# Performance work log

Hardware: AMD Instinct MI355X
Metric: run time of the kernel (lower is better)

The kernel has to match this reference:

```python
import jax, jax.numpy as jnp
from jax import lax
import numpy as np

NH = 4                      # num_heads in CrossScaleCom
KS = [3, 5, 7, 9]           # per-head depthwise kernel sizes
WS = 2                      # window_size in LocalFeatureGuided
GGM_K = 7                   # guide-token generator kernel size


def _dwconv(x, w, stride, pad):
    # depthwise conv: w has shape (C, 1, k, k), feature_group_count = C
    return lax.conv_general_dilated(
        x, w, (stride, stride), [(pad, pad), (pad, pad)],
        feature_group_count=x.shape[1],
        dimension_numbers=("NCHW", "OIHW", "NCHW"))


def _forward(x, dw_w0, dw_b0, dw_w1, dw_b1, dw_w2, dw_b2, dw_w3, dw_b3,
             csc_w, csc_b, bn_gamma, bn_beta, bn_mean, bn_var,
             ggm_w, ggm_b, qkv_w, qkv_b, proj_w, proj_b):
    B, C, H, W = x.shape
    cph = C // NH
    # ---- CrossScaleCom: per-head multi-scale depthwise convs ----
    xh = x.reshape(B, NH, cph, H, W)
    dws = [(dw_w0, dw_b0), (dw_w1, dw_b1), (dw_w2, dw_b2), (dw_w3, dw_b3)]
    heads = [_dwconv(xh[:, i], w, 1, KS[i] // 2) + b[None, :, None, None]
             for i, (w, b) in enumerate(dws)]
    y = jnp.stack(heads, 1)                      # (B, NH, cph, H, W)
    y = y.transpose(0, 2, 1, 3, 4).reshape(B, C, H, W)  # channel shuffle
    y = jnp.einsum("bchw,oc->bohw", y, csc_w) + csc_b[None, :, None, None]
    Co = y.shape[1]
    # ---- LocalFeatureGuided ----
    # ggm: BatchNorm (eval) -> GELU (exact) -> depthwise conv k=7 stride=WS
    inv = bn_gamma / jnp.sqrt(bn_var + 1e-5)
    g = (y - bn_mean[None, :, None, None]) * inv[None, :, None, None] \
        + bn_beta[None, :, None, None]
    g = jax.nn.gelu(g, approximate=False)
    g = _dwconv(g, ggm_w, WS, GGM_K // 2) + ggm_b[None, :, None, None]  # (B,Co,Ho,Wo)
    Ho, Wo = H // WS, W // WS
    L = Ho * Wo
    # unfold(kernel=WS, stride=WS) -> (B, Co, WS*WS, L), torch unfold ordering
    xu = y.reshape(B, Co, Ho, WS, Wo, WS).transpose(0, 1, 3, 5, 2, 4)
    xu = xu.reshape(B, Co, WS * WS, L)
    tokens = jnp.concatenate([g.reshape(B, Co, 1, L), xu], axis=2)  # (B,Co,5,L)
    # 1x1 conv over channel dim == einsum
    qkv = jnp.einsum("bcpl,oc->bopl", tokens, qkv_w) + qkv_b[None, :, None, None]
    q, k, v = jnp.split(qkv, 3, axis=1)          # each (B, Co, 5, L)
    # tiny 5x5 attention per (batch, channel), contracting over windows L
    attn = jnp.einsum("bcpl,bcql->bcpq", q, k) / (Co ** 0.5)
    attn = jax.nn.softmax(attn, axis=-1)
    out = jnp.einsum("bcpq,bcql->bcpl", attn, v)  # (B, Co, 5, L)
    out = out[:, :, 0, :].reshape(B, Co, Ho, Wo)  # guide-token output
    out = jnp.einsum("bchw,oc->bohw", out, proj_w) + proj_b[None, :, None, None]
    return out


def setup_inputs() -> dict:
    key = jax.random.key(0)
    ks = jax.random.split(key, 16)
    B, Cin, Cout, H, W = 8, 64, 128, 224, 224
    cph = Cin // NH
    s = 0.05
    d = {"x": jax.random.normal(ks[0], (B, Cin, H, W), jnp.float32)}
    for i, kk in enumerate(KS):
        d[f"dw_w{i}"] = jax.random.normal(ks[1 + i], (cph, 1, kk, kk), jnp.float32) * s
        d[f"dw_b{i}"] = jnp.zeros((cph,), jnp.float32)
    d["csc_w"] = jax.random.normal(ks[5], (Cout, Cin), jnp.float32) * s
    d["csc_b"] = jnp.zeros((Cout,), jnp.float32)
    d["bn_gamma"] = jnp.ones((Cout,), jnp.float32)
    d["bn_beta"] = jnp.zeros((Cout,), jnp.float32)
    d["bn_mean"] = jnp.zeros((Cout,), jnp.float32)
    d["bn_var"] = jnp.ones((Cout,), jnp.float32)
    d["ggm_w"] = jax.random.normal(ks[6], (Cout, 1, GGM_K, GGM_K), jnp.float32) * s
    d["ggm_b"] = jnp.zeros((Cout,), jnp.float32)
    d["qkv_w"] = jax.random.normal(ks[7], (3 * Cout, Cout), jnp.float32) * s
    d["qkv_b"] = jnp.zeros((3 * Cout,), jnp.float32)
    d["proj_w"] = jax.random.normal(ks[8], (Cout, Cout), jnp.float32) * s
    d["proj_b"] = jnp.zeros((Cout,), jnp.float32)
    return d


def reference(x, dw_w0, dw_b0, dw_w1, dw_b1, dw_w2, dw_b2, dw_w3, dw_b3,
              csc_w, csc_b, bn_gamma, bn_beta, bn_mean, bn_var,
              ggm_w, ggm_b, qkv_w, qkv_b, proj_w, proj_b):
    return _forward(x, dw_w0, dw_b0, dw_w1, dw_b1, dw_w2, dw_b2, dw_w3, dw_b3,
                    csc_w, csc_b, bn_gamma, bn_beta, bn_mean, bn_var,
                    ggm_w, ggm_b, qkv_w, qkv_b, proj_w, proj_b)
```

## Files before the change

kernel.cpp:

```cpp
#include <hip/hip_runtime.h>

#define BB 8
#define CIN 64
#define CO 128
#define Hdim 224
#define Wdim 224
#define HWt (224*224)
#define HO 112
#define WO 112
#define Lt (112*112)

typedef unsigned short u16;
typedef short bf16x8 __attribute__((ext_vector_type(8)));
typedef float f32x4  __attribute__((ext_vector_type(4)));
#define MFMA16(a,b,c) __builtin_amdgcn_mfma_f32_16x16x32_bf16((a),(b),(c),0,0,0)

__device__ inline u16 f2bf(float f) {
    union { float f; unsigned u; } v; v.f = f;
    unsigned r = (v.u + 0x7fffu + ((v.u >> 16) & 1u)) >> 16;
    return (u16)r;
}
__device__ inline float bf2f(u16 h) {
    union { unsigned u; float f; } v; v.u = ((unsigned)h) << 16; return v.f;
}
__device__ inline float uasf(unsigned u) {
    union { unsigned u; float f; } v; v.u = u; return v.f;
}
__device__ inline float sum8bf(uint4 v) {
    return bf2f(v.x & 0xffff) + bf2f(v.x >> 16) + bf2f(v.y & 0xffff) + bf2f(v.y >> 16)
         + bf2f(v.z & 0xffff) + bf2f(v.z >> 16) + bf2f(v.w & 0xffff) + bf2f(v.w >> 16);
}

__device__ inline float gelu_fast(float x) {
    float z  = x * 0.7071067811865476f;
    float az = fabsf(z);
    float t  = __builtin_amdgcn_rcpf(fmaf(0.3275911f, az, 1.0f));
    float p  = fmaf(fmaf(fmaf(fmaf(1.061405429f, t, -1.453152027f), t,
                    1.421413741f), t, -0.284496736f), t, 0.254829592f);
    float e  = __expf(-z * z);
    float er = copysignf(1.0f - p * t * e, z);
    return 0.5f * x * (1.0f + er);
}

template<int HEAD>
__global__ __launch_bounds__(256) void dw_conv(
    const float* __restrict__ x, const float* __restrict__ w,
    const float* __restrict__ bias, u16* __restrict__ dwb)
{
    constexpr int K   = 3 + 2*HEAD;
    constexpr int PAD = HEAD + 1;
    constexpr int R   = 32 + 2*PAD;
    const int tile = blockIdx.x;
    const int c    = blockIdx.y;
    const int b    = blockIdx.z;
    const int th = (tile/7)*32, tw = (tile%7)*32;
    __shared__ float patch[R*40];
    const int tid = threadIdx.x;
    const float* xin = x + (size_t)(b*CIN + HEAD*16 + c)*HWt;
    for (int idx = tid; idx < R*40; idx += 256) {
        int r = idx / 40, cc = idx - r*40;
        int gy = th - PAD + r, gx = tw - 4 + cc;
        float v = 0.f;
        if (gy >= 0 && gy < Hdim && gx >= 0 && gx < Wdim) v = xin[gy*Wdim + gx];
        patch[idx] = v;
    }
    float wreg[K*K];
    const float* wp = w + c*K*K;
    #pragma unroll
    for (int i = 0; i < K*K; i++) wreg[i] = wp[i];
    const float bv = bias[c];
    __syncthreads();

    const int ty = tid >> 3, x0 = (tid & 7) * 4;
    float acc[4] = {bv, bv, bv, bv};
    #pragma unroll
    for (int ky = 0; ky < K; ky++) {
        float rr[12];
        *(float4*)&rr[0] = *(const float4*)&patch[(ty+ky)*40 + x0];
        *(float4*)&rr[4] = *(const float4*)&patch[(ty+ky)*40 + x0 + 4];
        *(float4*)&rr[8] = *(const float4*)&patch[(ty+ky)*40 + x0 + 8];
        #pragma unroll
        for (int kx = 0; kx < K; kx++) {
            const float wv = wreg[ky*K + kx];
            #pragma unroll
            for (int j = 0; j < 4; j++)
                acc[j] = fmaf(rr[j + kx + 4 - PAD], wv, acc[j]);
        }
    }
    const int s = c*4 + HEAD;
    u16 o4[4] = {f2bf(acc[0]), f2bf(acc[1]), f2bf(acc[2]), f2bf(acc[3])};
    *(uint2*)&dwb[(size_t)(b*CIN + s)*HWt + (th+ty)*Wdim + tw + x0] = *(uint2*)o4;
}

__global__ __launch_bounds__(256) void csc_mfma(
    const float* __restrict__ W, const float* __restrict__ bias,
    const u16* __restrict__ dwb, u16* __restrict__ y4)
{
    const int b  = blockIdx.z;
    const int p0 = blockIdx.x * 128;
    __shared__ u16 Abuf[128*72];
    __shared__ u16 Tbuf[32*132];
    const int tid = threadIdx.x;
    const int wv = tid >> 6, ln = tid & 63;
    const int mh = (wv >> 1)*64, nh = (wv & 1)*64;
    const int lm = ln & 15, kq = ln >> 4;
    for (int t = tid; t < 1024; t += 256) {
        int r = t >> 3, kk = (t & 7)*8;
        const float* src = &W[r*64 + kk];
        float4 f0 = *(const float4*)src, f1 = *(const float4*)(src+4);
        u16 tmp[8] = {f2bf(f0.x),f2bf(f0.y),f2bf(f0.z),f2bf(f0.w),
                      f2bf(f1.x),f2bf(f1.y),f2bf(f1.z),f2bf(f1.w)};
        *(uint4*)&Abuf[r*72 + kk] = *(uint4*)tmp;
    }
    const u16* Db = dwb + (size_t)b*CIN*HWt;
    f32x4 acc[4][4];
    #pragma unroll
    for (int i=0;i<4;i++)
        #pragma unroll
        for (int j=0;j<4;j++) acc[i][j] = (f32x4){0.f,0.f,0.f,0.f};

    for (int kc = 0; kc < 64; kc += 32) {
        __syncthreads();
        for (int t = tid; t < 512; t += 256) {
            int k = t >> 4, n0 = (t & 15)*8;
            *(uint4*)&Tbuf[k*132 + n0] = *(const uint4*)&Db[(size_t)(kc+k)*HWt + p0 + n0];
        }
        __syncthreads();
        bf16x8 af[4], bfr[4];
        #pragma unroll
        for (int tm=0;tm<4;tm++)
            af[tm] = *(bf16x8*)&Abuf[(mh + tm*16 + lm)*72 + kc + kq*8];
        #pragma unroll
        for (int tn=0;tn<4;tn++) {
            int n = nh + tn*16 + lm;
            #pragma unroll
            for (int j=0;j<8;j++) bfr[tn][j] = (short)Tbuf[(kq*8+j)*132 + n];
        }
        #pragma unroll
        for (int tm=0;tm<4;tm++)
            #pragma unroll
            for (int tn=0;tn<4;tn++)
                acc[tm][tn] = MFMA16(af[tm], bfr[tn], acc[tm][tn]);
    }
    #pragma unroll
    for (int tm=0;tm<4;tm++) {
        #pragma unroll
        for (int r=0;r<4;r++) {
            int o = mh + tm*16 + kq*4 + r;
            float bb = bias[o];
            #pragma unroll
            for (int tn=0;tn<4;tn++) {
                int p = p0 + nh + tn*16 + lm;
                int gy = p / 224, gx = p - gy*224;
                int w = (gy&1)*2 + (gx&1);
                y4[((size_t)(b*CO + o)*4 + w)*Lt + (gy>>1)*WO + (gx>>1)]
                    = f2bf(acc[tm][tn][r] + bb);
            }
        }
    }
}

__global__ __launch_bounds__(256) void ggm_kernel(const u16* __restrict__ y4,
    const float* __restrict__ gamma, const float* __restrict__ beta,
    const float* __restrict__ mean, const float* __restrict__ var,
    const float* __restrict__ gw, const float* __restrict__ gb,
    u16* __restrict__ gbf)
{
    const int ho0 = blockIdx.x * 16;
    const int c   = blockIdx.y;
    const int b   = blockIdx.z;
    __shared__ float patch[37*240];
    const int tid = threadIdx.x;

    const float inv = gamma[c] * rsqrtf(var[c] + 1e-5f);
    const float bsh = fmaf(-mean[c], inv, beta[c]);
    const u16* ybc = y4 + (size_t)(b*CO + c)*4*Lt;

    float wk[49];
    const float* wp = gw + c*49;
    #pragma unroll
    for (int i = 0; i < 49; i++) wk[i] = wp[i];
    const float bv = gb[c];

    for (int idx = tid; idx < 37*60; idx += 256) {
        int r = idx / 60, j = idx - r*60;
        int gy = 2*ho0 - 3 + r;
        float4 v = make_float4(0.f, 0.f, 0.f, 0.f);
        if (gy >= 0 && gy < Hdim && j >= 2 && j <= 57) {
            const u16* pe = ybc + (size_t)((gy&1)*2)*Lt + (gy>>1)*WO + (2*j - 4);
            unsigned e = *(const unsigned*)pe;
            unsigned o = *(const unsigned*)(pe + Lt);
            v.x = gelu_fast(fmaf(uasf(e << 16),         inv, bsh));
            v.y = gelu_fast(fmaf(uasf(o << 16),         inv, bsh));
            v.z = gelu_fast(fmaf(uasf(e & 0xffff0000u), inv, bsh));
            v.w = gelu_fast(fmaf(uasf(o & 0xffff0000u), inv, bsh));
        }
        *(float4*)&patch[idx*4] = v;
    }
    __syncthreads();

    if (tid < 224) {
        const int n = tid % 56;
        const int g = tid / 56;
        float acc[4][2];
        #pragma unroll
        for (int i = 0; i < 4; i++) { acc[i][0] = bv; acc[i][1] = bv; }
        #pragma unroll
        for (int rr = 0; rr < 13; rr++) {
            const float* row = &patch[(8*g + rr)*240 + 4*n + 4];
            float f[12];
            *(float4*)&f[0] = *(const float4*)&row[0];
            *(float4*)&f[4] = *(const float4*)&row[4];
            *(float4*)&f[8] = *(const float4*)&row[8];
            #pragma unroll
            for (int i = 0; i < 4; i++) {
                const int ky = rr - 2*i;
                if (ky >= 0 && ky <= 6) {
                    #pragma unroll
                    for (int kx = 0; kx < 7; kx++) {
                        const float wv = wk[ky*7 + kx];
                        acc[i][0] = fmaf(f[kx + 1], wv, acc[i][0]);
                        acc[i][1] = fmaf(f[kx + 3], wv, acc[i][1]);
                    }
                }
            }
        }
        u16* gout = gbf + (size_t)(b*CO + c)*Lt;
        #pragma unroll
        for (int i = 0; i < 4; i++) {
            u16 o2[2] = {f2bf(acc[i][0]), f2bf(acc[i][1])};
            *(unsigned*)&gout[(ho0 + 4*g + i)*WO + 2*n] = *(unsigned*)o2;
        }
    }
}

__global__ __launch_bounds__(256) void G_mfma(
    const u16* __restrict__ gbf, const u16* __restrict__ y4,
    float* __restrict__ Gpart)
{
    const int b = blockIdx.z, p = blockIdx.y, split = blockIdx.x;
    const u16* Ab = gbf + (size_t)b*CO*Lt;
    const u16* Bb; int brs;
    if (p == 0) { Bb = Ab; brs = Lt; }
    else        { Bb = y4 + ((size_t)b*CO*4 + (p-1))*Lt; brs = 4*Lt; }
    __shared__ u16 Abuf[128*72];
    __shared__ u16 Bbuf[128*72];
    const int tid = threadIdx.x;
    const int wv = tid >> 6, ln = tid & 63;
    const int mh = (wv >> 1)*64, nh = (wv & 1)*64;
    const int lm = ln & 15, kq = ln >> 4;
    f32x4 acc[4][4];
    #pragma unroll
    for (int i=0;i<4;i++)
        #pragma unroll
        for (int j=0;j<4;j++) acc[i][j] = (f32x4){0.f,0.f,0.f,0.f};

    for (int ci = split; ci < 196; ci += 16) {
        const int l0 = ci*64;
        __syncthreads();
        for (int t = tid; t < 1024; t += 256) {
            int r = t >> 3, kk = (t & 7)*8;
            *(uint4*)&Abuf[r*72 + kk] = *(const uint4*)&Ab[(size_t)r*Lt  + l0 + kk];
            *(uint4*)&Bbuf[r*72 + kk] = *(const uint4*)&Bb[(size_t)r*brs + l0 + kk];
        }
        __syncthreads();
        #pragma unroll
        for (int ks = 0; ks < 2; ks++) {
            bf16x8 af[4], bfr[4];
            #pragma unroll
            for (int tm=0;tm<4;tm++)
                af[tm]  = *(bf16x8*)&Abuf[(mh + tm*16 + lm)*72 + ks*32 + kq*8];
            #pragma unroll
            for (int tn=0;tn<4;tn++)
                bfr[tn] = *(bf16x8*)&Bbuf[(nh + tn*16 + lm)*72 + ks*32 + kq*8];
            #pragma unroll
            for (int tm=0;tm<4;tm++)
                #pragma unroll
                for (int tn=0;tn<4;tn++)
                    acc[tm][tn] = MFMA16(af[tm], bfr[tn], acc[tm][tn]);
        }
    }
    float* Go = Gpart + ((size_t)(split*40) + b*5 + p)*CO*CO;
    #pragma unroll
    for (int tm=0;tm<4;tm++)
        #pragma unroll
        for (int r=0;r<4;r++) {
            int mrow = mh + tm*16 + kq*4 + r;
            #pragma unroll
            for (int tn=0;tn<4;tn++)
                Go[mrow*CO + nh + tn*16 + lm] = acc[tm][tn][r];
        }
}

__global__ void G_reduce(const float* __restrict__ Gpart, float* __restrict__ G)
{
    const int bp = blockIdx.x;
    const int i4 = (blockIdx.y*256 + threadIdx.x)*4;
    float4 s = make_float4(0.f, 0.f, 0.f, 0.f);
    #pragma unroll
    for (int sp = 0; sp < 16; sp++) {
        float4 v = *(const float4*)&Gpart[((size_t)(sp*40) + bp)*CO*CO + i4];
        s.x += v.x; s.y += v.y; s.z += v.z; s.w += v.w;
    }
    *(float4*)&G[(size_t)bp*CO*CO + i4] = s;
}

__global__ void S_kernel(const u16* __restrict__ gbf, const u16* __restrict__ y4,
                         float* __restrict__ S)
{
    const int b = blockIdx.x >> 7, c = blockIdx.x & 127;
    const u16* gr = gbf + (size_t)(b*CO+c)*Lt;
    const u16* yr = y4  + (size_t)(b*CO+c)*4*Lt;
    float vals[5] = {0.f,0.f,0.f,0.f,0.f};
    for (int i = threadIdx.x*8; i < Lt; i += 256*8)
        vals[0] += sum8bf(*(const uint4*)&gr[i]);
    #pragma unroll
    for (int w=0; w<4; w++)
        for (int i = threadIdx.x*8; i < Lt; i += 256*8)
            vals[1+w] += sum8bf(*(const uint4*)&yr[(size_t)w*Lt + i]);
    #pragma unroll
    for (int off=32; off>0; off>>=1) {
        #pragma unroll
        for (int q=0;q<5;q++) vals[q] += __shfl_down(vals[q], off);
    }
    __shared__ float red[4][5];
    const int wid = threadIdx.x>>6, lane = threadIdx.x&63;
    if (lane==0) {
        #pragma unroll
        for (int q=0;q<5;q++) red[wid][q] = vals[q];
    }
    __syncthreads();
    if (threadIdx.x==0) {
        #pragma unroll
        for (int q=0;q<5;q++)
            S[((size_t)b*5 + q)*CO + c] = red[0][q]+red[1][q]+red[2][q]+red[3][q];
    }
}

__global__ __launch_bounds__(256) void fused_logits_kernel(
    const float* __restrict__ G, const float* __restrict__ S,
    const float* __restrict__ qkv_w, const float* __restrict__ qkv_b,
    float* __restrict__ lg)
{
    const int p = blockIdx.x, b = blockIdx.y;
    __shared__ float Wl[32*132];
    __shared__ float Al[32*132];
    __shared__ float KGl[128*128];
    const int tid = threadIdx.x;
    const int og = (tid >> 4) * 8;
    const int pg = (tid & 15) * 8;
    const float* Gp = G + (size_t)(b*5 + p)*CO*CO;
    float acc[8][8];
    #pragma unroll
    for (int i=0;i<8;i++)
        #pragma unroll
        for (int j=0;j<8;j++) acc[i][j]=0.f;

    for (int kc = 0; kc < 128; kc += 32) {
        __syncthreads();
        for (int t = tid; t < 4096; t += 256) {
            int kk = t & 31, o = t >> 5;
            Wl[kk*132 + o] = Gp[(size_t)o*CO + kc + kk];
            Al[kk*132 + o] = qkv_w[(size_t)(CO + o)*CO + kc + kk];
        }
        __syncthreads();
        #pragma unroll 4
        for (int kk = 0; kk < 32; kk++) {
            float wv[8], av[8];
            *(float4*)&wv[0] = *(const float4*)&Wl[kk*132+og];
            *(float4*)&wv[4] = *(const float4*)&Wl[kk*132+og+4];
            *(float4*)&av[0] = *(const float4*)&Al[kk*132+pg];
            *(float4*)&av[4] = *(const float4*)&Al[kk*132+pg+4];
            #pragma unroll
            for (int i=0;i<8;i++)
                #pragma unroll
                for (int j=0;j<8;j++)
                    acc[i][j] = fmaf(wv[i], av[j], acc[i][j]);
        }
    }
    #pragma unroll
    for (int i=0;i<8;i++) {
        #pragma unroll
        for (int j=0;j<8;j+=4)
            *(float4*)&KGl[(og+i)*128 + pg + j] = *(float4*)&acc[i][j];
    }
    __syncthreads();
    if (tid < 128) {
        const int c = tid;
        const float qb = qkv_b[c], kb = qkv_b[CO + c];
        const float* S0 = S + (size_t)b*5*CO;
        const float* Sp = S0 + p*CO;
        const float* qwrow = qkv_w + (size_t)c*CO;
        const float* kwrow = qkv_w + (size_t)(CO + c)*CO;
        float sq = qb * 12544.f, ks = 0.f, s = 0.f;
        for (int c2 = 0; c2 < CO; c2++) {
            sq = fmaf(qwrow[c2], S0[c2], sq);
            ks = fmaf(kwrow[c2], Sp[c2], ks);
            s  = fmaf(qwrow[c2], KGl[c2*128 + c], s);
        }
        lg[(size_t)(b*5 + p)*CO + c] = s + qb*ks + kb*sq;
    }
}

__global__ void softmax5_kernel(const float* __restrict__ lg, float* __restrict__ a)
{
    const int b = blockIdx.x, c = threadIdx.x;
    float v[5];
    #pragma unroll
    for (int p=0;p<5;p++) v[p] = lg[(size_t)(b*5 + p)*CO + c];
    const float scl = 0.08838834764831845f;
    float mx = v[0];
    #pragma unroll
    for (int p=1;p<5;p++) mx = fmaxf(mx, v[p]);
    float e[5], sum = 0.f;
    #pragma unroll
    for (int p=0;p<5;p++){ e[p] = __expf((v[p]-mx)*scl); sum += e[p]; }
    const float rs = 1.f/sum;
    #pragma unroll
    for (int p=0;p<5;p++) a[((size_t)b*CO + c)*5 + p] = e[p]*rs;
}

__global__ void F_kernel(const float* __restrict__ proj_w,
    const float* __restrict__ qkv_w, const float* __restrict__ a,
    float* __restrict__ F)
{
    const int b = blockIdx.z, p = blockIdx.y;
    const int o  = blockIdx.x*2 + (threadIdx.x>>7);
    const int cp = threadIdx.x & 127;
    const float* vw = qkv_w + 2*CO*CO;
    float s = 0.f;
    for (int c=0;c<CO;c++)
        s = fmaf(proj_w[o*CO+c] * a[((size_t)b*CO+c)*5 + p], vw[c*CO+cp], s);
    F[(((size_t)(b*5+p))*CO + o)*CO + cp] = s;
}

__global__ void bias_kernel(const float* __restrict__ proj_w,
    const float* __restrict__ proj_b, const float* __restrict__ qkv_b,
    float* __restrict__ biasout)
{
    const int o = threadIdx.x;
    const float* vb = qkv_b + 2*CO;
    float s = proj_b[o];
    for (int c=0;c<CO;c++) s = fmaf(proj_w[o*CO+c], vb[c], s);
    biasout[o] = s;
}

__global__ __launch_bounds__(256) void final_mfma(
    const float* __restrict__ F, const u16* __restrict__ gbf,
    const u16* __restrict__ y4, const float* __restrict__ biasout,
    float* __restrict__ out)
{
    const int b = blockIdx.z;
    const int p0 = blockIdx.x * 128;
    __shared__ u16 Abuf[128*40];
    __shared__ u16 Tbuf[32*132];
    const int tid = threadIdx.x;
    const int wv = tid >> 6, ln = tid & 63;
    const int mh = (wv >> 1)*64, nh = (wv & 1)*64;
    const int lm = ln & 15, kq = ln >> 4;
    f32x4 acc[4][4];
    #pragma unroll
    for (int i=0;i<4;i++)
        #pragma unroll
        for (int j=0;j<4;j++) acc[i][j] = (f32x4){0.f,0.f,0.f,0.f};

    for (int ph = 0; ph < 5; ph++) {
        const float* Fp = F + (size_t)(b*5 + ph)*CO*CO;
        const u16* Bb; int brs;
        if (ph == 0) { Bb = gbf + (size_t)b*CO*Lt; brs = Lt; }
        else         { Bb = y4 + ((size_t)b*CO*4 + (ph-1))*Lt; brs = 4*Lt; }
        for (int kc = 0; kc < CO; kc += 32) {
            __syncthreads();
            for (int t = tid; t < 512; t += 256) {
                int r = t >> 2, kk = (t & 3)*8;
                const float* src = &Fp[r*CO + kc + kk];
                float4 f0 = *(const float4*)src, f1 = *(const float4*)(src+4);
                u16 tmp[8] = {f2bf(f0.x),f2bf(f0.y),f2bf(f0.z),f2bf(f0.w),
                              f2bf(f1.x),f2bf(f1.y),f2bf(f1.z),f2bf(f1.w)};
                *(uint4*)&Abuf[r*40 + kk] = *(uint4*)tmp;
            }
            for (int t = tid; t < 512; t += 256) {
                int k = t >> 4, n0 = (t & 15)*8;
                *(uint4*)&Tbuf[k*132 + n0] = *(const uint4*)&Bb[(size_t)(kc+k)*brs + p0 + n0];
            }
            __syncthreads();
            bf16x8 af[4], bfr[4];
            #pragma unroll
            for (int tm=0;tm<4;tm++)
                af[tm] = *(bf16x8*)&Abuf[(mh + tm*16 + lm)*40 + kq*8];
            #pragma unroll
            for (int tn=0;tn<4;tn++) {
                int n = nh + tn*16 + lm;
                #pragma unroll
                for (int j=0;j<8;j++) bfr[tn][j] = (short)Tbuf[(kq*8+j)*132 + n];
            }
            #pragma unroll
            for (int tm=0;tm<4;tm++)
                #pragma unroll
                for (int tn=0;tn<4;tn++)
                    acc[tm][tn] = MFMA16(af[tm], bfr[tn], acc[tm][tn]);
        }
    }
    float* Ob = out + (size_t)b*CO*Lt;
    #pragma unroll
    for (int tm=0;tm<4;tm++) {
        #pragma unroll
        for (int r=0;r<4;r++) {
            int o = mh + tm*16 + kq*4 + r;
            float bb = biasout[o];
            #pragma unroll
            for (int tn=0;tn<4;tn++)
                Ob[(size_t)o*Lt + p0 + nh + tn*16 + lm] = acc[tm][tn][r] + bb;
        }
    }
}

extern "C" void kernel_launch(void* const* d_in, const int* in_sizes, int n_in,
                              void* d_out, int out_size, void* d_ws, size_t ws_size,
                              hipStream_t stream) {
    const float* x      = (const float*)d_in[0];
    const float* dw_w0  = (const float*)d_in[1];
    const float* dw_b0  = (const float*)d_in[2];
    const float* dw_w1  = (const float*)d_in[3];
    const float* dw_b1  = (const float*)d_in[4];
    const float* dw_w2  = (const float*)d_in[5];
    const float* dw_b2  = (const float*)d_in[6];
    const float* dw_w3  = (const float*)d_in[7];
    const float* dw_b3  = (const float*)d_in[8];
    const float* csc_w  = (const float*)d_in[9];
    const float* csc_b  = (const float*)d_in[10];
    const float* bn_g   = (const float*)d_in[11];
    const float* bn_b   = (const float*)d_in[12];
    const float* bn_m   = (const float*)d_in[13];
    const float* bn_v   = (const float*)d_in[14];
    const float* ggm_w  = (const float*)d_in[15];
    const float* ggm_b  = (const float*)d_in[16];
    const float* qkv_w  = (const float*)d_in[17];
    const float* qkv_b  = (const float*)d_in[18];
    const float* proj_w = (const float*)d_in[19];
    const float* proj_b = (const float*)d_in[20];
    float* out = (float*)d_out;

    char* ws = (char*)d_ws;
    u16*   y4  = (u16*)(ws);
    u16*   dwb = (u16*)(ws + 102760448);
    u16*   gbf = (u16*)(ws + 154140672);
    float* G   = (float*)(ws + 179830784);
    float* lgb = G  + 655360;
    float* F   = lgb + 5120;
    float* S   = F  + 655360;
    float* aw  = S  + 5120;
    float* bo  = aw + 5120;
    float* Gpart = (float*)(ws + 102760448);

    dw_conv<0><<<dim3(49, 16, 8), 256, 0, stream>>>(x, dw_w0, dw_b0, dwb);
    dw_conv<1><<<dim3(49, 16, 8), 256, 0, stream>>>(x, dw_w1, dw_b1, dwb);
    dw_conv<2><<<dim3(49, 16, 8), 256, 0, stream>>>(x, dw_w2, dw_b2, dwb);
    dw_conv<3><<<dim3(49, 16, 8), 256, 0, stream>>>(x, dw_w3, dw_b3, dwb);

    csc_mfma<<<dim3(392, 1, 8), 256, 0, stream>>>(csc_w, csc_b, dwb, y4);

    ggm_kernel<<<dim3(7, 128, 8), 256, 0, stream>>>(
        y4, bn_g, bn_b, bn_m, bn_v, ggm_w, ggm_b, gbf);

    G_mfma<<<dim3(16, 5, 8), 256, 0, stream>>>(gbf, y4, Gpart);
    G_reduce<<<dim3(40, 16), 256, 0, stream>>>(Gpart, G);

    S_kernel<<<dim3(1024), 256, 0, stream>>>(gbf, y4, S);

    fused_logits_kernel<<<dim3(5, 8), 256, 0, stream>>>(G, S, qkv_w, qkv_b, lgb);

    softmax5_kernel<<<dim3(8), 128, 0, stream>>>(lgb, aw);

    F_kernel<<<dim3(64, 5, 8), 256, 0, stream>>>(proj_w, qkv_w, aw, F);
    bias_kernel<<<dim3(1), 128, 0, stream>>>(proj_w, proj_b, qkv_b, bo);

    final_mfma<<<dim3(98, 1, 8), 256, 0, stream>>>(F, gbf, y4, bo, out);
}
```

Before: 626.4 us.

## Fuse BN+GELU into csc epilogue, fold S sums into G_mfma, store F in bf16

The csc GEMM epilogue now also writes a BN+GELU-activated copy of y4 (gf4) when the workspace is large enough, so the ggm conv kernel reads activated values instead of recomputing GELU per tap. The separate S_kernel reduction is removed: row sums are computed inside G_mfma by an extra MFMA against a ones vector and reduced in G_reduce. F_kernel writes bf16 directly, so final_mfma no longer converts from fp32. This costs an extra 51MB write of gf4 and adds MFMA work on half the waves, in exchange for removing a full-tensor read pass and repeated GELU evaluation.

```diff
diff --git a/kernel.cpp b/kernel.cpp
--- a/kernel.cpp
+++ b/kernel.cpp
@@ -25,10 +25,6 @@
 }
 __device__ inline float uasf(unsigned u) {
     union { unsigned u; float f; } v; v.u = u; return v.f;
-}
-__device__ inline float sum8bf(uint4 v) {
-    return bf2f(v.x & 0xffff) + bf2f(v.x >> 16) + bf2f(v.y & 0xffff) + bf2f(v.y >> 16)
-         + bf2f(v.z & 0xffff) + bf2f(v.z >> 16) + bf2f(v.w & 0xffff) + bf2f(v.w >> 16);
 }
 
 __device__ inline float gelu_fast(float x) {
@@ -94,7 +90,10 @@
 
 __global__ __launch_bounds__(256) void csc_mfma(
     const float* __restrict__ W, const float* __restrict__ bias,
-    const u16* __restrict__ dwb, u16* __restrict__ y4)
+    const u16* __restrict__ dwb, u16* __restrict__ y4,
+    const float* __restrict__ gamma, const float* __restrict__ beta,
+    const float* __restrict__ mean, const float* __restrict__ var,
+    u16* __restrict__ gf4)
 {
     const int b  = blockIdx.z;
     const int p0 = blockIdx.x * 128;
@@ -148,19 +147,96 @@
         for (int r=0;r<4;r++) {
             int o = mh + tm*16 + kq*4 + r;
             float bb = bias[o];
+            float inv = 0.f, bsh = 0.f;
+            if (gf4) {
+                inv = gamma[o] * rsqrtf(var[o] + 1e-5f);
+                bsh = fmaf(-mean[o], inv, beta[o]);
+            }
             #pragma unroll
             for (int tn=0;tn<4;tn++) {
                 int p = p0 + nh + tn*16 + lm;
                 int gy = p / 224, gx = p - gy*224;
                 int w = (gy&1)*2 + (gx&1);
-                y4[((size_t)(b*CO + o)*4 + w)*Lt + (gy>>1)*WO + (gx>>1)]
-                    = f2bf(acc[tm][tn][r] + bb);
-            }
-        }
-    }
-}
-
-__global__ __launch_bounds__(256) void ggm_kernel(const u16* __restrict__ y4,
+                size_t idx = ((size_t)(b*CO + o)*4 + w)*Lt + (gy>>1)*WO + (gx>>1);
+                float t = acc[tm][tn][r] + bb;
+                y4[idx] = f2bf(t);
+                if (gf4)
+                    gf4[idx] = f2bf(gelu_fast(fmaf(t, inv, bsh)));
+            }
+        }
+    }
+}
+
+__global__ __launch_bounds__(256) void ggm_pre(const u16* __restrict__ gf4,
+    const float* __restrict__ gw, const float* __restrict__ gb,
+    u16* __restrict__ gbf)
+{
+    const int ho0 = blockIdx.x * 16;
+    const int c   = blockIdx.y;
+    const int b   = blockIdx.z;
+    __shared__ float patch[37*240];
+    const int tid = threadIdx.x;
+    const u16* gbc = gf4 + (size_t)(b*CO + c)*4*Lt;
+
+    float wk[49];
+    const float* wp = gw + c*49;
+    #pragma unroll
+    for (int i = 0; i < 49; i++) wk[i] = wp[i];
+    const float bv = gb[c];
+
+    for (int idx = tid; idx < 37*60; idx += 256) {
+        int r = idx / 60, j = idx - r*60;
+        int gy = 2*ho0 - 3 + r;
+        float4 v = make_float4(0.f, 0.f, 0.f, 0.f);
+        if (gy >= 0 && gy < Hdim && j >= 2 && j <= 57) {
+            const u16* pe = gbc + (size_t)((gy&1)*2)*Lt + (gy>>1)*WO + (2*j - 4);
+            unsigned e = *(const unsigned*)pe;
+            unsigned o = *(const unsigned*)(pe + Lt);
+            v.x = uasf(e << 16);
+            v.y = uasf(o << 16);
+            v.z = uasf(e & 0xffff0000u);
+            v.w = uasf(o & 0xffff0000u);
+        }
+        *(float4*)&patch[idx*4] = v;
+    }
+    __syncthreads();
+
+    if (tid < 224) {
+        const int n = tid % 56;
+        const int g = tid / 56;
+        float acc[4][2];
+        #pragma unroll
+        for (int i = 0; i < 4; i++) { acc[i][0] = bv; acc[i][1] = bv; }
+        #pragma unroll
+        for (int rr = 0; rr < 13; rr++) {
+            const float* row = &patch[(8*g + rr)*240 + 4*n + 4];
+            float f[12];
+            *(float4*)&f[0] = *(const float4*)&row[0];
+            *(float4*)&f[4] = *(const float4*)&row[4];
+            *(float4*)&f[8] = *(const float4*)&row[8];
+            #pragma unroll
+            for (int i = 0; i < 4; i++) {
+                const int ky = rr - 2*i;
+                if (ky >= 0 && ky <= 6) {
+                    #pragma unroll
+                    for (int kx = 0; kx < 7; kx++) {
+                        const float wv = wk[ky*7 + kx];
+                        acc[i][0] = fmaf(f[kx + 1], wv, acc[i][0]);
+                        acc[i][1] = fmaf(f[kx + 3], wv, acc[i][1]);
+                    }
+                }
+            }
+        }
+        u16* gout = gbf + (size_t)(b*CO + c)*Lt;
+        #pragma unroll
+        for (int i = 0; i < 4; i++) {
+            u16 o2[2] = {f2bf(acc[i][0]), f2bf(acc[i][1])};
+            *(unsigned*)&gout[(ho0 + 4*g + i)*WO + 2*n] = *(unsigned*)o2;
+        }
+    }
+}
+
+__global__ __launch_bounds__(256) void ggm_gelu(const u16* __restrict__ y4,
     const float* __restrict__ gamma, const float* __restrict__ beta,
     const float* __restrict__ mean, const float* __restrict__ var,
     const float* __restrict__ gw, const float* __restrict__ gb,
@@ -236,7 +312,7 @@
 
 __global__ __launch_bounds__(256) void G_mfma(
     const u16* __restrict__ gbf, const u16* __restrict__ y4,
-    float* __restrict__ Gpart)
+    float* __restrict__ Gpart, float* __restrict__ Spart)
 {
     const int b = blockIdx.z, p = blockIdx.y, split = blockIdx.x;
     const u16* Ab = gbf + (size_t)b*CO*Lt;
@@ -254,6 +330,13 @@
     for (int i=0;i<4;i++)
         #pragma unroll
         for (int j=0;j<4;j++) acc[i][j] = (f32x4){0.f,0.f,0.f,0.f};
+    bf16x8 af_s;
+    #pragma unroll
+    for (int j=0;j<8;j++) af_s[j] = (lm == 0) ? (short)0x3F80 : (short)0;
+    f32x4 acc_s[4];
+    #pragma unroll
+    for (int j=0;j<4;j++) acc_s[j] = (f32x4){0.f,0.f,0.f,0.f};
+    const bool sWave = (mh == 0);
 
     for (int ci = split; ci < 196; ci += 16) {
         const int l0 = ci*64;
@@ -278,6 +361,11 @@
                 #pragma unroll
                 for (int tn=0;tn<4;tn++)
                     acc[tm][tn] = MFMA16(af[tm], bfr[tn], acc[tm][tn]);
+            if (sWave) {
+                #pragma unroll
+                for (int tn=0;tn<4;tn++)
+                    acc_s[tn] = MFMA16(af_s, bfr[tn], acc_s[tn]);
+            }
         }
     }
     float* Go = Gpart + ((size_t)(split*40) + b*5 + p)*CO*CO;
@@ -290,9 +378,17 @@
             for (int tn=0;tn<4;tn++)
                 Go[mrow*CO + nh + tn*16 + lm] = acc[tm][tn][r];
         }
-}
-
-__global__ void G_reduce(const float* __restrict__ Gpart, float* __restrict__ G)
+    if (sWave && kq == 0) {
+        float* So = Spart + ((size_t)(split*40) + b*5 + p)*CO;
+        #pragma unroll
+        for (int tn=0;tn<4;tn++)
+            So[nh + tn*16 + lm] = acc_s[tn][0];
+    }
+}
+
+__global__ void G_reduce(const float* __restrict__ Gpart,
+                         const float* __restrict__ Spart,
+                         float* __restrict__ G, float* __restrict__ S)
 {
     const int bp = blockIdx.x;
     const int i4 = (blockIdx.y*256 + threadIdx.x)*4;
@@ -303,37 +399,12 @@
         s.x += v.x; s.y += v.y; s.z += v.z; s.w += v.w;
     }
     *(float4*)&G[(size_t)bp*CO*CO + i4] = s;
-}
-
-__global__ void S_kernel(const u16* __restrict__ gbf, const u16* __restrict__ y4,
-                         float* __restrict__ S)
-{
-    const int b = blockIdx.x >> 7, c = blockIdx.x & 127;
-    const u16* gr = gbf + (size_t)(b*CO+c)*Lt;
-    const u16* yr = y4  + (size_t)(b*CO+c)*4*Lt;
-    float vals[5] = {0.f,0.f,0.f,0.f,0.f};
-    for (int i = threadIdx.x*8; i < Lt; i += 256*8)
-        vals[0] += sum8bf(*(const uint4*)&gr[i]);
-    #pragma unroll
-    for (int w=0; w<4; w++)
-        for (int i = threadIdx.x*8; i < Lt; i += 256*8)
-            vals[1+w] += sum8bf(*(const uint4*)&yr[(size_t)w*Lt + i]);
-    #pragma unroll
-    for (int off=32; off>0; off>>=1) {
-        #pragma unroll
-        for (int q=0;q<5;q++) vals[q] += __shfl_down(vals[q], off);
-    }
-    __shared__ float red[4][5];
-    const int wid = threadIdx.x>>6, lane = threadIdx.x&63;
-    if (lane==0) {
-        #pragma unroll
-        for (int q=0;q<5;q++) red[wid][q] = vals[q];
-    }
-    __syncthreads();
-    if (threadIdx.x==0) {
-        #pragma unroll
-        for (int q=0;q<5;q++)
-            S[((size_t)b*5 + q)*CO + c] = red[0][q]+red[1][q]+red[2][q]+red[3][q];
+    if (blockIdx.y == 0 && threadIdx.x < CO) {
+        float ss = 0.f;
+        #pragma unroll
+        for (int sp = 0; sp < 16; sp++)
+            ss += Spart[((size_t)(sp*40) + bp)*CO + threadIdx.x];
+        S[(size_t)bp*CO + threadIdx.x] = ss;
     }
 }
 
@@ -422,7 +493,7 @@
 
 __global__ void F_kernel(const float* __restrict__ proj_w,
     const float* __restrict__ qkv_w, const float* __restrict__ a,
-    float* __restrict__ F)
+    u16* __restrict__ Fb)
 {
     const int b = blockIdx.z, p = blockIdx.y;
     const int o  = blockIdx.x*2 + (threadIdx.x>>7);
@@ -431,7 +502,7 @@
     float s = 0.f;
     for (int c=0;c<CO;c++)
         s = fmaf(proj_w[o*CO+c] * a[((size_t)b*CO+c)*5 + p], vw[c*CO+cp], s);
-    F[(((size_t)(b*5+p))*CO + o)*CO + cp] = s;
+    Fb[(((size_t)(b*5+p))*CO + o)*CO + cp] = f2bf(s);
 }
 
 __global__ void bias_kernel(const float* __restrict__ proj_w,
@@ -446,7 +517,7 @@
 }
 
 __global__ __launch_bounds__(256) void final_mfma(
-    const float* __restrict__ F, const u16* __restrict__ gbf,
+    const u16* __restrict__ Fb, const u16* __restrict__ gbf,
     const u16* __restrict__ y4, const float* __restrict__ biasout,
     float* __restrict__ out)
 {
@@ -465,7 +536,7 @@
         for (int j=0;j<4;j++) acc[i][j] = (f32x4){0.f,0.f,0.f,0.f};
 
     for (int ph = 0; ph < 5; ph++) {
-        const float* Fp = F + (size_t)(b*5 + ph)*CO*CO;
+        const u16* Fp = Fb + (size_t)(b*5 + ph)*CO*CO;
         const u16* Bb; int brs;
         if (ph == 0) { Bb = gbf + (size_t)b*CO*Lt; brs = Lt; }
         else         { Bb = y4 + ((size_t)b*CO*4 + (ph-1))*Lt; brs = 4*Lt; }
@@ -473,11 +544,7 @@
             __syncthreads();
             for (int t = tid; t < 512; t += 256) {
                 int r = t >> 2, kk = (t & 3)*8;
-                const float* src = &Fp[r*CO + kc + kk];
-                float4 f0 = *(const float4*)src, f1 = *(const float4*)(src+4);
-                u16 tmp[8] = {f2bf(f0.x),f2bf(f0.y),f2bf(f0.z),f2bf(f0.w),
-                              f2bf(f1.x),f2bf(f1.y),f2bf(f1.z),f2bf(f1.w)};
-                *(uint4*)&Abuf[r*40 + kk] = *(uint4*)tmp;
+                *(uint4*)&Abuf[r*40 + kk] = *(const uint4*)&Fp[r*CO + kc + kk];
             }
             for (int t = tid; t < 512; t += 256) {
                 int k = t >> 4, n0 = (t & 15)*8;
@@ -546,34 +613,40 @@
     u16*   dwb = (u16*)(ws + 102760448);
     u16*   gbf = (u16*)(ws + 154140672);
     float* G   = (float*)(ws + 179830784);
-    float* lgb = G  + 655360;
-    float* F   = lgb + 5120;
-    float* S   = F  + 655360;
-    float* aw  = S  + 5120;
-    float* bo  = aw + 5120;
+    float* lgb = (float*)(ws + 182452224);
+    u16*   Fb  = (u16*)  (ws + 182472704);
+    float* S   = (float*)(ws + 183783424);
+    float* aw  = (float*)(ws + 183803904);
+    float* bo  = (float*)(ws + 183824384);
     float* Gpart = (float*)(ws + 102760448);
+    float* Spart = (float*)(ws + 144703488);
+    u16*   gf4 = (u16*)(ws + 183824896);
+    const bool big = ws_size >= (size_t)286585344;
 
     dw_conv<0><<<dim3(49, 16, 8), 256, 0, stream>>>(x, dw_w0, dw_b0, dwb);
     dw_conv<1><<<dim3(49, 16, 8), 256, 0, stream>>>(x, dw_w1, dw_b1, dwb);
     dw_conv<2><<<dim3(49, 16, 8), 256, 0, stream>>>(x, dw_w2, dw_b2, dwb);
     dw_conv<3><<<dim3(49, 16, 8), 256, 0, stream>>>(x, dw_w3, dw_b3, dwb);
 
-    csc_mfma<<<dim3(392, 1, 8), 256, 0, stream>>>(csc_w, csc_b, dwb, y4);
-
-    ggm_kernel<<<dim3(7, 128, 8), 256, 0, stream>>>(
-        y4, bn_g, bn_b, bn_m, bn_v, ggm_w, ggm_b, gbf);
-
-    G_mfma<<<dim3(16, 5, 8), 256, 0, stream>>>(gbf, y4, Gpart);
-    G_reduce<<<dim3(40, 16), 256, 0, stream>>>(Gpart, G);
-
-    S_kernel<<<dim3(1024), 256, 0, stream>>>(gbf, y4, S);
+    csc_mfma<<<dim3(392, 1, 8), 256, 0, stream>>>(
+        csc_w, csc_b, dwb, y4, bn_g, bn_b, bn_m, bn_v, big ? gf4 : (u16*)nullptr);
+
+    if (big) {
+        ggm_pre<<<dim3(7, 128, 8), 256, 0, stream>>>(gf4, ggm_w, ggm_b, gbf);
+    } else {
+        ggm_gelu<<<dim3(7, 128, 8), 256, 0, stream>>>(
+            y4, bn_g, bn_b, bn_m, bn_v, ggm_w, ggm_b, gbf);
+    }
+
+    G_mfma<<<dim3(16, 5, 8), 256, 0, stream>>>(gbf, y4, Gpart, Spart);
+    G_reduce<<<dim3(40, 16), 256, 0, stream>>>(Gpart, Spart, G, S);
 
     fused_logits_kernel<<<dim3(5, 8), 256, 0, stream>>>(G, S, qkv_w, qkv_b, lgb);
 
     softmax5_kernel<<<dim3(8), 128, 0, stream>>>(lgb, aw);
 
-    F_kernel<<<dim3(64, 5, 8), 256, 0, stream>>>(proj_w, qkv_w, aw, F);
+    F_kernel<<<dim3(64, 5, 8), 256, 0, stream>>>(proj_w, qkv_w, aw, Fb);
     bias_kernel<<<dim3(1), 128, 0, stream>>>(proj_w, proj_b, qkv_b, bo);
 
-    final_mfma<<<dim3(98, 1, 8), 256, 0, stream>>>(F, gbf, y4, bo, out);
-}
+    final_mfma<<<dim3(98, 1, 8), 256, 0, stream>>>(Fb, gbf, y4, bo, out);
+}
```

After: 684.4 us. +9.3%, slower.
